# Kernel tuning notes

Hardware: AMD Instinct MI355X
Metric: run time of the kernel (lower is better)

## Reference

```python
import jax, jax.numpy as jnp
import numpy as np

SQRT_DIM = np.sqrt(64.0).astype(np.float32)
NEG_INF = -1000000000.0


def setup_inputs() -> dict:
    key = jax.random.key(0)
    kq, kk, kv = jax.random.split(key, 3)
    B, H, S, D = 4, 8, 2048, 64
    q = jax.random.normal(kq, (B, H, S, D), dtype=jnp.float32)
    k = jax.random.normal(kk, (B, H, S, D), dtype=jnp.float32)
    v = jax.random.normal(kv, (B, H, S, D), dtype=jnp.float32)
    mask = jnp.ones((B, 1, S, S), dtype=jnp.int32)
    return {"q": q, "k": k, "v": v, "mask": mask}


def reference(q, k, v, mask):
    # scores: [B, H, S, S]
    attn = jnp.einsum("bhqd,bhkd->bhqk", q, k) / SQRT_DIM
    attn = jnp.where(mask == 0, NEG_INF, attn)
    attn = jax.nn.softmax(attn, axis=-1)
    # dropout p=0.0 -> identity
    output = jnp.einsum("bhqk,bhkd->bhqd", attn, v)
    return (output, attn)
```

## Files before the change

### kernel.cpp

```cpp
#include <hip/hip_runtime.h>
#include <hip/hip_bf16.h>
#include <stdint.h>

#define NB 4
#define NH 8
#define SDIM 2048
#define DDIM 64

typedef short s8v __attribute__((ext_vector_type(8)));
typedef float f4v __attribute__((ext_vector_type(4)));

__device__ __forceinline__ float bf2f(unsigned short h) {
    union { unsigned int u; float f; } c; c.u = ((unsigned int)h) << 16; return c.f;
}
__device__ __forceinline__ unsigned short f2bf(float x) {
    union { float f; unsigned int u; } c; c.f = x;
    return (unsigned short)((c.u + 0x7FFFu + ((c.u >> 16) & 1u)) >> 16);
}

__global__ void sdpa_prep_cast_k(const float* __restrict__ k, unsigned short* __restrict__ kb) {
    int i = blockIdx.x * 256 + threadIdx.x;
    float4 v = ((const float4*)k)[i];
    ushort4 o;
    o.x = f2bf(v.x * 0.125f);
    o.y = f2bf(v.y * 0.125f);
    o.z = f2bf(v.z * 0.125f);
    o.w = f2bf(v.w * 0.125f);
    ((ushort4*)kb)[i] = o;
}

__global__ void sdpa_prep_transpose_v(const float* __restrict__ v, unsigned short* __restrict__ vt) {
    __shared__ float t[64][65];
    const int bh = blockIdx.x >> 5;
    const int kt = blockIdx.x & 31;
    const int tid = threadIdx.x;
    const float* src = v + ((size_t)bh * SDIM + (size_t)kt * 64) * DDIM;
    #pragma unroll
    for (int i = 0; i < 4; ++i) {
        int idx = i * 256 + tid;
        int kl = idx >> 4, c4 = idx & 15;
        float4 val = ((const float4*)(src + kl * DDIM))[c4];
        t[kl][c4 * 4 + 0] = val.x; t[kl][c4 * 4 + 1] = val.y;
        t[kl][c4 * 4 + 2] = val.z; t[kl][c4 * 4 + 3] = val.w;
    }
    __syncthreads();
    const int d   = tid >> 2;
    const int klb = (tid & 3) << 4;
    unsigned short* dst = vt + ((size_t)bh * DDIM + d) * SDIM + kt * 64 + klb;
    #pragma unroll
    for (int c = 0; c < 4; ++c) {
        ushort4 w;
        w.x = f2bf(t[klb + c * 4 + 0][d]);
        w.y = f2bf(t[klb + c * 4 + 1][d]);
        w.z = f2bf(t[klb + c * 4 + 2][d]);
        w.w = f2bf(t[klb + c * 4 + 3][d]);
        ((ushort4*)dst)[c] = w;
    }
}

__launch_bounds__(256, 2)
__global__ void sdpa_main(const float* __restrict__ q,
                          const unsigned short* __restrict__ kb,
                          const unsigned short* __restrict__ vtb,
                          const int* __restrict__ mask,
                          float* __restrict__ outO,
                          float* __restrict__ outP) {
    extern __shared__ char lds[];
    unsigned short* sc = (unsigned short*)lds;

    const int bx = blockIdx.x;
    const int bh = bx >> 7;
    const int q0 = (bx & 127) << 4;
    const int b  = bh >> 3;

    const int tid  = threadIdx.x;
    const int wave = tid >> 6;
    const int lane = tid & 63;
    const int l15  = lane & 15;
    const int quad = lane >> 4;

    s8v aq0, aq1;
    {
        const float* qr = q + ((size_t)bh * SDIM + q0 + l15) * DDIM + quad * 8;
        float4 x0 = ((const float4*)qr)[0];
        float4 x1 = ((const float4*)qr)[1];
        float4 y0 = ((const float4*)(qr + 32))[0];
        float4 y1 = ((const float4*)(qr + 32))[1];
        aq0[0]=(short)f2bf(x0.x); aq0[1]=(short)f2bf(x0.y); aq0[2]=(short)f2bf(x0.z); aq0[3]=(short)f2bf(x0.w);
        aq0[4]=(short)f2bf(x1.x); aq0[5]=(short)f2bf(x1.y); aq0[6]=(short)f2bf(x1.z); aq0[7]=(short)f2bf(x1.w);
        aq1[0]=(short)f2bf(y0.x); aq1[1]=(short)f2bf(y0.y); aq1[2]=(short)f2bf(y0.z); aq1[3]=(short)f2bf(y0.w);
        aq1[4]=(short)f2bf(y1.x); aq1[5]=(short)f2bf(y1.y); aq1[6]=(short)f2bf(y1.z); aq1[7]=(short)f2bf(y1.w);
    }

    {
        const unsigned short* kbase = kb + (size_t)bh * SDIM * DDIM;
        const int n_start = wave << 9;
        #pragma unroll 2
        for (int t = 0; t < 32; ++t) {
            const int n0 = n_start + (t << 4);
            const unsigned short* krow = kbase + (size_t)(n0 + l15) * DDIM + quad * 8;
            s8v b0 = *(const s8v*)(krow);
            s8v b1 = *(const s8v*)(krow + 32);
            f4v acc = {0.f, 0.f, 0.f, 0.f};
            acc = __builtin_amdgcn_mfma_f32_16x16x32_bf16(aq0, b0, acc, 0, 0, 0);
            acc = __builtin_amdgcn_mfma_f32_16x16x32_bf16(aq1, b1, acc, 0, 0, 0);
            const int col = n0 + l15;
            const int blk = col >> 3;
            const int off = col & 7;
            #pragma unroll
            for (int r = 0; r < 4; ++r) {
                int row = quad * 4 + r;
                sc[row * 2048 + (((blk ^ row) << 3) | off)] = f2bf(acc[r]);
            }
        }
    }
    __syncthreads();

    const int row = tid >> 4;
    const int l16 = tid & 15;
    unsigned short* scrow = sc + row * 2048;
    const int* mrow = mask + (size_t)b * SDIM * SDIM + (size_t)(q0 + row) * SDIM;

    float rmax = -3.0e38f;
    for (int i = 0; i < 16; ++i) {
        int j = l16 + (i << 4);
        unsigned short* p = scrow + (((j ^ row) << 3));
        s8v vv = *(s8v*)p;
        int4 m0 = ((const int4*)mrow)[j * 2 + 0];
        int4 m1 = ((const int4*)mrow)[j * 2 + 1];
        int mm[8] = { m0.x, m0.y, m0.z, m0.w, m1.x, m1.y, m1.z, m1.w };
        #pragma unroll
        for (int e = 0; e < 8; ++e) {
            float s = bf2f((unsigned short)vv[e]);
            s = (mm[e] == 0) ? -1.0e9f : s;
            rmax = fmaxf(rmax, s);
            vv[e] = (short)f2bf(s);
        }
        *(s8v*)p = vv;
    }
    #pragma unroll
    for (int d = 1; d < 16; d <<= 1) rmax = fmaxf(rmax, __shfl_xor(rmax, d));

    float rsum = 0.f;
    for (int i = 0; i < 16; ++i) {
        int j = l16 + (i << 4);
        unsigned short* p = scrow + (((j ^ row) << 3));
        s8v vv = *(s8v*)p;
        #pragma unroll
        for (int e = 0; e < 8; ++e) {
            float ex = __expf(bf2f((unsigned short)vv[e]) - rmax);
            rsum += ex;
            vv[e] = (short)f2bf(ex);
        }
        *(s8v*)p = vv;
    }
    #pragma unroll
    for (int d = 1; d < 16; d <<= 1) rsum += __shfl_xor(rsum, d);
    const float rinv = 1.0f / rsum;

    {
        float* prow = outP + (size_t)bh * SDIM * SDIM + (size_t)(q0 + row) * SDIM;
        for (int i = 0; i < 16; ++i) {
            int j = l16 + (i << 4);
            unsigned short* p = scrow + (((j ^ row) << 3));
            s8v vv = *(s8v*)p;
            float e0 = bf2f((unsigned short)vv[0]) * rinv;
            float e1 = bf2f((unsigned short)vv[1]) * rinv;
            float e2 = bf2f((unsigned short)vv[2]) * rinv;
            float e3 = bf2f((unsigned short)vv[3]) * rinv;
            float e4 = bf2f((unsigned short)vv[4]) * rinv;
            float e5 = bf2f((unsigned short)vv[5]) * rinv;
            float e6 = bf2f((unsigned short)vv[6]) * rinv;
            float e7 = bf2f((unsigned short)vv[7]) * rinv;
            float4 o0 = { e0, e1, e2, e3 };
            float4 o1 = { e4, e5, e6, e7 };
            ((float4*)prow)[j * 2 + 0] = o0;
            ((float4*)prow)[j * 2 + 1] = o1;
            vv[0]=(short)f2bf(e0); vv[1]=(short)f2bf(e1); vv[2]=(short)f2bf(e2); vv[3]=(short)f2bf(e3);
            vv[4]=(short)f2bf(e4); vv[5]=(short)f2bf(e5); vv[6]=(short)f2bf(e6); vv[7]=(short)f2bf(e7);
            *(s8v*)p = vv;
        }
    }
    __syncthreads();

    {
        const unsigned short* vbase = vtb + ((size_t)bh * DDIM + (wave << 4) + l15) * SDIM + quad * 8;
        unsigned short* arow = sc + l15 * 2048;
        f4v acc0 = {0,0,0,0}, acc1 = {0,0,0,0}, acc2 = {0,0,0,0}, acc3 = {0,0,0,0};
        #pragma unroll 4
        for (int ks = 0; ks < 64; ++ks) {
            const int k0 = ks << 5;
            s8v a  = *(const s8v*)(arow + ((((k0 >> 3) + quad) ^ l15) << 3));
            s8v bb = *(const s8v*)(vbase + k0);
            if ((ks & 3) == 0)      acc0 = __builtin_amdgcn_mfma_f32_16x16x32_bf16(a, bb, acc0, 0, 0, 0);
            else if ((ks & 3) == 1) acc1 = __builtin_amdgcn_mfma_f32_16x16x32_bf16(a, bb, acc1, 0, 0, 0);
            else if ((ks & 3) == 2) acc2 = __builtin_amdgcn_mfma_f32_16x16x32_bf16(a, bb, acc2, 0, 0, 0);
            else                    acc3 = __builtin_amdgcn_mfma_f32_16x16x32_bf16(a, bb, acc3, 0, 0, 0);
        }
        f4v acc = acc0 + acc1 + acc2 + acc3;
        float* orow = outO + ((size_t)bh * SDIM + q0) * DDIM + (wave << 4) + l15;
        #pragma unroll
        for (int r = 0; r < 4; ++r)
            orow[(quad * 4 + r) * DDIM] = acc[r];
    }
}

extern "C" void kernel_launch(void* const* d_in, const int* in_sizes, int n_in,
                              void* d_out, int out_size, void* d_ws, size_t ws_size,
                              hipStream_t stream) {
    const float* q  = (const float*)d_in[0];
    const float* k  = (const float*)d_in[1];
    const float* v  = (const float*)d_in[2];
    const int* mask = (const int*)d_in[3];

    const size_t qkv_elems = (size_t)NB * NH * SDIM * DDIM;
    float* outO = (float*)d_out;
    float* outP = (float*)d_out + qkv_elems;

    unsigned short* kb  = (unsigned short*)d_ws;
    unsigned short* vtb = kb + qkv_elems;

    sdpa_prep_cast_k<<<(int)(qkv_elems / 1024), 256, 0, stream>>>(k, kb);
    sdpa_prep_transpose_v<<<NB * NH * (SDIM / 64), 256, 0, stream>>>(v, vtb);
    sdpa_main<<<NB * NH * (SDIM / 16), 256, 65536, stream>>>(q, kb, vtb, mask, outO, outP);
}
```

Baseline: 899.9 us.

## Double block threads, keep softmax rows in registers, split PV over K

Doubles the block to 512 threads. Each row is now handled by 32 lanes, and its scores stay in a 64-float register array instead of being read and rewritten in LDS on every softmax pass. The log2(e)/8 factor is folded into the K cast so exp2f can replace __expf. P is written with nontemporal stores. The PV product is split across two K halves, with a partial-sum reduction through LDS. The trade-off is a tighter register budget: the stricter launch bounds plus the 64-entry array may cause spills, and there is an extra barrier for the reduction.

```diff
diff --git a/kernel.cpp b/kernel.cpp
--- a/kernel.cpp
+++ b/kernel.cpp
@@ -7,6 +7,8 @@
 #define SDIM 2048
 #define DDIM 64
 
+#define KSCALE 0.18033688011112042f
+
 typedef short s8v __attribute__((ext_vector_type(8)));
 typedef float f4v __attribute__((ext_vector_type(4)));
 
@@ -22,10 +24,10 @@
     int i = blockIdx.x * 256 + threadIdx.x;
     float4 v = ((const float4*)k)[i];
     ushort4 o;
-    o.x = f2bf(v.x * 0.125f);
-    o.y = f2bf(v.y * 0.125f);
-    o.z = f2bf(v.z * 0.125f);
-    o.w = f2bf(v.w * 0.125f);
+    o.x = f2bf(v.x * KSCALE);
+    o.y = f2bf(v.y * KSCALE);
+    o.z = f2bf(v.z * KSCALE);
+    o.w = f2bf(v.w * KSCALE);
     ((ushort4*)kb)[i] = o;
 }
 
@@ -58,7 +60,7 @@
     }
 }
 
-__launch_bounds__(256, 2)
+__launch_bounds__(512, 4)
 __global__ void sdpa_main(const float* __restrict__ q,
                           const unsigned short* __restrict__ kb,
                           const unsigned short* __restrict__ vtb,
@@ -94,9 +96,9 @@
 
     {
         const unsigned short* kbase = kb + (size_t)bh * SDIM * DDIM;
-        const int n_start = wave << 9;
+        const int n_start = wave << 8;
         #pragma unroll 2
-        for (int t = 0; t < 32; ++t) {
+        for (int t = 0; t < 16; ++t) {
             const int n0 = n_start + (t << 4);
             const unsigned short* krow = kbase + (size_t)(n0 + l15) * DDIM + quad * 8;
             s8v b0 = *(const s8v*)(krow);
@@ -116,92 +118,94 @@
     }
     __syncthreads();
 
-    const int row = tid >> 4;
-    const int l16 = tid & 15;
+    const int row = tid >> 5;
+    const int l32 = tid & 31;
     unsigned short* scrow = sc + row * 2048;
     const int* mrow = mask + (size_t)b * SDIM * SDIM + (size_t)(q0 + row) * SDIM;
 
+    float s[64];
     float rmax = -3.0e38f;
-    for (int i = 0; i < 16; ++i) {
-        int j = l16 + (i << 4);
-        unsigned short* p = scrow + (((j ^ row) << 3));
-        s8v vv = *(s8v*)p;
+    #pragma unroll
+    for (int i = 0; i < 8; ++i) {
+        const int j = l32 + (i << 5);
+        s8v vv = *(const s8v*)(scrow + ((j ^ row) << 3));
         int4 m0 = ((const int4*)mrow)[j * 2 + 0];
         int4 m1 = ((const int4*)mrow)[j * 2 + 1];
-        int mm[8] = { m0.x, m0.y, m0.z, m0.w, m1.x, m1.y, m1.z, m1.w };
+        const int mm[8] = { m0.x, m0.y, m0.z, m0.w, m1.x, m1.y, m1.z, m1.w };
         #pragma unroll
         for (int e = 0; e < 8; ++e) {
-            float s = bf2f((unsigned short)vv[e]);
-            s = (mm[e] == 0) ? -1.0e9f : s;
-            rmax = fmaxf(rmax, s);
-            vv[e] = (short)f2bf(s);
-        }
-        *(s8v*)p = vv;
-    }
-    #pragma unroll
-    for (int d = 1; d < 16; d <<= 1) rmax = fmaxf(rmax, __shfl_xor(rmax, d));
+            float x = bf2f((unsigned short)vv[e]);
+            x = (mm[e] == 0) ? -1.0e9f : x;
+            s[i * 8 + e] = x;
+            rmax = fmaxf(rmax, x);
+        }
+    }
+    #pragma unroll
+    for (int d = 1; d < 32; d <<= 1) rmax = fmaxf(rmax, __shfl_xor(rmax, d));
 
     float rsum = 0.f;
-    for (int i = 0; i < 16; ++i) {
-        int j = l16 + (i << 4);
-        unsigned short* p = scrow + (((j ^ row) << 3));
-        s8v vv = *(s8v*)p;
+    #pragma unroll
+    for (int i = 0; i < 64; ++i) {
+        float e = exp2f(s[i] - rmax);
+        s[i] = e;
+        rsum += e;
+    }
+    #pragma unroll
+    for (int d = 1; d < 32; d <<= 1) rsum += __shfl_xor(rsum, d);
+    const float rinv = 1.0f / rsum;
+
+    {
+        float* prow = outP + (size_t)bh * SDIM * SDIM + (size_t)(q0 + row) * SDIM;
         #pragma unroll
-        for (int e = 0; e < 8; ++e) {
-            float ex = __expf(bf2f((unsigned short)vv[e]) - rmax);
-            rsum += ex;
-            vv[e] = (short)f2bf(ex);
-        }
-        *(s8v*)p = vv;
-    }
-    #pragma unroll
-    for (int d = 1; d < 16; d <<= 1) rsum += __shfl_xor(rsum, d);
-    const float rinv = 1.0f / rsum;
-
-    {
-        float* prow = outP + (size_t)bh * SDIM * SDIM + (size_t)(q0 + row) * SDIM;
-        for (int i = 0; i < 16; ++i) {
-            int j = l16 + (i << 4);
-            unsigned short* p = scrow + (((j ^ row) << 3));
-            s8v vv = *(s8v*)p;
-            float e0 = bf2f((unsigned short)vv[0]) * rinv;
-            float e1 = bf2f((unsigned short)vv[1]) * rinv;
-            float e2 = bf2f((unsigned short)vv[2]) * rinv;
-            float e3 = bf2f((unsigned short)vv[3]) * rinv;
-            float e4 = bf2f((unsigned short)vv[4]) * rinv;
-            float e5 = bf2f((unsigned short)vv[5]) * rinv;
-            float e6 = bf2f((unsigned short)vv[6]) * rinv;
-            float e7 = bf2f((unsigned short)vv[7]) * rinv;
-            float4 o0 = { e0, e1, e2, e3 };
-            float4 o1 = { e4, e5, e6, e7 };
-            ((float4*)prow)[j * 2 + 0] = o0;
-            ((float4*)prow)[j * 2 + 1] = o1;
-            vv[0]=(short)f2bf(e0); vv[1]=(short)f2bf(e1); vv[2]=(short)f2bf(e2); vv[3]=(short)f2bf(e3);
-            vv[4]=(short)f2bf(e4); vv[5]=(short)f2bf(e5); vv[6]=(short)f2bf(e6); vv[7]=(short)f2bf(e7);
-            *(s8v*)p = vv;
+        for (int i = 0; i < 8; ++i) {
+            const int j = l32 + (i << 5);
+            float p0 = s[i*8+0] * rinv, p1 = s[i*8+1] * rinv;
+            float p2 = s[i*8+2] * rinv, p3 = s[i*8+3] * rinv;
+            float p4 = s[i*8+4] * rinv, p5 = s[i*8+5] * rinv;
+            float p6 = s[i*8+6] * rinv, p7 = s[i*8+7] * rinv;
+            f4v o0 = { p0, p1, p2, p3 };
+            f4v o1 = { p4, p5, p6, p7 };
+            __builtin_nontemporal_store(o0, (f4v*)prow + j * 2 + 0);
+            __builtin_nontemporal_store(o1, (f4v*)prow + j * 2 + 1);
+            s8v vv;
+            vv[0]=(short)f2bf(p0); vv[1]=(short)f2bf(p1); vv[2]=(short)f2bf(p2); vv[3]=(short)f2bf(p3);
+            vv[4]=(short)f2bf(p4); vv[5]=(short)f2bf(p5); vv[6]=(short)f2bf(p6); vv[7]=(short)f2bf(p7);
+            *(s8v*)(scrow + ((j ^ row) << 3)) = vv;
         }
     }
     __syncthreads();
 
     {
-        const unsigned short* vbase = vtb + ((size_t)bh * DDIM + (wave << 4) + l15) * SDIM + quad * 8;
-        unsigned short* arow = sc + l15 * 2048;
-        f4v acc0 = {0,0,0,0}, acc1 = {0,0,0,0}, acc2 = {0,0,0,0}, acc3 = {0,0,0,0};
+        const int dt = wave & 3;
+        const int kh = wave >> 2;
+        const unsigned short* vbase = vtb + ((size_t)bh * DDIM + (dt << 4) + l15) * SDIM
+                                          + (kh << 10) + quad * 8;
+        const unsigned short* arow = sc + l15 * 2048;
+        f4v acc0 = {0,0,0,0}, acc1 = {0,0,0,0};
         #pragma unroll 4
-        for (int ks = 0; ks < 64; ++ks) {
-            const int k0 = ks << 5;
+        for (int ks = 0; ks < 32; ++ks) {
+            const int k0 = (kh << 10) + (ks << 5);
             s8v a  = *(const s8v*)(arow + ((((k0 >> 3) + quad) ^ l15) << 3));
-            s8v bb = *(const s8v*)(vbase + k0);
-            if ((ks & 3) == 0)      acc0 = __builtin_amdgcn_mfma_f32_16x16x32_bf16(a, bb, acc0, 0, 0, 0);
-            else if ((ks & 3) == 1) acc1 = __builtin_amdgcn_mfma_f32_16x16x32_bf16(a, bb, acc1, 0, 0, 0);
-            else if ((ks & 3) == 2) acc2 = __builtin_amdgcn_mfma_f32_16x16x32_bf16(a, bb, acc2, 0, 0, 0);
-            else                    acc3 = __builtin_amdgcn_mfma_f32_16x16x32_bf16(a, bb, acc3, 0, 0, 0);
-        }
-        f4v acc = acc0 + acc1 + acc2 + acc3;
-        float* orow = outO + ((size_t)bh * SDIM + q0) * DDIM + (wave << 4) + l15;
-        #pragma unroll
-        for (int r = 0; r < 4; ++r)
-            orow[(quad * 4 + r) * DDIM] = acc[r];
+            s8v bb = *(const s8v*)(vbase + (ks << 5));
+            if (ks & 1) acc1 = __builtin_amdgcn_mfma_f32_16x16x32_bf16(a, bb, acc1, 0, 0, 0);
+            else        acc0 = __builtin_amdgcn_mfma_f32_16x16x32_bf16(a, bb, acc0, 0, 0, 0);
+        }
+        f4v acc = acc0 + acc1;
+
+        __syncthreads();
+        float* scratch = (float*)lds;
+        if (kh == 1) {
+            #pragma unroll
+            for (int r = 0; r < 4; ++r)
+                scratch[(dt << 8) + ((quad * 4 + r) << 4) + l15] = acc[r];
+        }
+        __syncthreads();
+        if (kh == 0) {
+            float* orow = outO + ((size_t)bh * SDIM + q0) * DDIM + (dt << 4) + l15;
+            #pragma unroll
+            for (int r = 0; r < 4; ++r)
+                orow[(quad * 4 + r) * DDIM] = acc[r] + scratch[(dt << 8) + ((quad * 4 + r) << 4) + l15];
+        }
     }
 }
 
@@ -222,5 +226,5 @@
 
     sdpa_prep_cast_k<<<(int)(qkv_elems / 1024), 256, 0, stream>>>(k, kb);
     sdpa_prep_transpose_v<<<NB * NH * (SDIM / 64), 256, 0, stream>>>(v, vtb);
-    sdpa_main<<<NB * NH * (SDIM / 16), 256, 65536, stream>>>(q, kb, vtb, mask, outO, outP);
-}
+    sdpa_main<<<NB * NH * (SDIM / 16), 512, 65536, stream>>>(q, kb, vtb, mask, outO, outP);
+}
```

Measured after the change: 865.2 us. 1.04x faster.
